# Performance work log

Measured on AMD Instinct MI355X. Metric: run time of the kernel, lower is better.

## Reference

```python
import jax, jax.numpy as jnp
import numpy as np

L = 8          # layers_num
G = 2 * L + 1  # grid side = 17
NH = 30        # n_hiper
D = 768
N = 4096       # ray samples


def setup_inputs() -> dict:
    key = jax.random.key(0)
    k1, k2, k3 = jax.random.split(key, 3)
    # coords must be in [-L, L) so shifted indices floor+1/ceil+1 stay in-bounds
    samples = jax.random.uniform(k1, (N, 3), minval=-float(L), maxval=float(L) - 1e-3)
    last_point = jax.random.uniform(k2, (3,), minval=-float(L), maxval=float(L) - 1e-3)
    embeddings = jax.random.normal(k3, (G, G, G, NH + 1, D), dtype=jnp.float32)
    return {"samples": samples, "last_point": last_point, "embeddings": embeddings}


def _interpolate(emb, samples):
    """Vectorized port of Text3DSpaceAll.interpolate for all N samples.
    emb: (G,G,G,NH+1,D); samples: (N,3). Returns (N, NH+1, D)."""
    Gs = emb.shape[0]
    p = samples + L                       # shift into [0, G-1)
    f = jnp.floor(p)
    c = jnp.ceil(p)
    d = p - f                             # fractional parts (same as pre-shift)
    fx, fy, fz = f[:, 0].astype(jnp.int32), f[:, 1].astype(jnp.int32), f[:, 2].astype(jnp.int32)
    cy, cz = c[:, 1].astype(jnp.int32), c[:, 2].astype(jnp.int32)
    dx, dy, dz = d[:, 0], d[:, 1], d[:, 2]

    def w(a):  # broadcast per-sample scalar over (NH+1, D)
        return a[:, None, None]

    def clip(i):
        return jnp.clip(i, 0, Gs - 1)

    def line(iy, iz):
        # 2-4 point stencil along x with boundary-dependent count
        g = lambda ix: emb[clip(ix), iy, iz]          # gather -> (N, NH+1, D)
        m_lo = (fx > 0).astype(dx.dtype)
        m_hi = (fx + 2 < Gs).astype(dx.dtype)
        out = (g(fx) * w(2.0 - dx) + g(fx + 1) * w(1.0 + dx)
               + g(fx - 1) * w((1.0 - dx) * m_lo)
               + g(fx + 2) * w(dx * m_hi))
        cnt = 2.0 + m_lo + m_hi
        return out / w(cnt)

    def plane(iz):
        m_lo = (fy > 0).astype(dy.dtype)
        m_hi = (fy + 2 < Gs).astype(dy.dtype)
        out = (line(fy, iz) * w(2.0 - dy) + line(cy, iz) * w(1.0 + dy)
               + line(clip(fy - 1), iz) * w((1.0 - dy) * m_lo)
               + line(clip(cy + 1), iz) * w(dy * m_hi))
        cnt = 2.0 + m_lo + m_hi
        return out / w(cnt)

    m_lo = (fz > 0).astype(dz.dtype)
    m_hi = (fz + 2 < Gs).astype(dz.dtype)
    out = (plane(fz) * w(2.0 - dz) + plane(cz) * w(1.0 + dz)
           + plane(clip(fz - 1)) * w((1.0 - dz) * m_lo)
           + plane(clip(cz + 1)) * w(dz * m_hi))
    cnt = 2.0 + m_lo + m_hi
    return out / w(cnt)


def reference(samples, last_point, embeddings):
    n_hiper = embeddings.shape[3] - 1
    interp = _interpolate(embeddings, samples)          # (N, NH+1, D)
    emb = interp[:, :n_hiper]                           # (N, NH, D)
    density = jax.nn.relu(interp[:, n_hiper])           # (N, D)
    # distance from each sample to the next (last one to last_point)
    nxt = jnp.concatenate([samples[1:], last_point[None]], axis=0)
    dists = jnp.linalg.norm(samples - nxt, axis=-1)     # (N,)
    sd = density * dists[:, None]                       # (N, D)
    # exclusive cumulative optical depth -> transmittance
    csum = jnp.cumsum(sd, axis=0)
    excl = jnp.concatenate([jnp.zeros_like(sd[:1]), csum[:-1]], axis=0)
    T = jnp.exp(-excl)
    alpha = 1.0 - jnp.exp(-sd)
    wgt = T * alpha                                     # (N, D)
    return jnp.einsum('nd,nhd->hd', wgt, emb)           # (NH, D)
```

## Files before the change

kernel.cpp:

```cpp
#include <hip/hip_runtime.h>
#include <math.h>

#define LL 8
#define G 17
#define NH 30
#define D 768
#define N 4096
#define CH 31
#define CELLS (G*G*G)
#define CSTRIDE (CH*D)
#define NBIN 16

__device__ __forceinline__ int iclip(int i){ return i<0?0:(i>G-1?G-1:i); }

__global__ void k_prep(const float* __restrict__ samples, const float* __restrict__ last_point,
                       float* __restrict__ wxyz, int* __restrict__ ixyz,
                       float* __restrict__ dist, int* __restrict__ sampleBin,
                       int* __restrict__ binCount){
    int s = blockIdx.x*blockDim.x + threadIdx.x;
    if (s >= N) return;
    float x0 = samples[s*3+0], y0 = samples[s*3+1], z0 = samples[s*3+2];
    float p[3] = {x0 + (float)LL, y0 + (float)LL, z0 + (float)LL};
    float fv[3], cv[3], dv[3]; int fi[3], ci[3];
    for (int a=0;a<3;a++){
        fv[a]=floorf(p[a]); cv[a]=ceilf(p[a]); dv[a]=p[a]-fv[a];
        fi[a]=(int)fv[a]; ci[a]=(int)cv[a];
    }
    {
        int fx=fi[0]; float dx=dv[0];
        float mlo=(fx>0)?1.f:0.f, mhi=(fx+2<G)?1.f:0.f;
        float cnt=2.f+mlo+mhi;
        float w[4]={(1.f-dx)*mlo/cnt,(2.f-dx)/cnt,(1.f+dx)/cnt,dx*mhi/cnt};
        int id[4]={iclip(fx-1),iclip(fx),iclip(fx+1),iclip(fx+2)};
        for(int i=0;i<4;i++){ wxyz[s*12+i]=w[i]; ixyz[s*12+i]=id[i]; }
    }
    {
        int fy=fi[1], cy=ci[1]; float dy=dv[1];
        float mlo=(fy>0)?1.f:0.f, mhi=(fy+2<G)?1.f:0.f;
        float cnt=2.f+mlo+mhi;
        float w[4]={(1.f-dy)*mlo/cnt,(2.f-dy)/cnt,(1.f+dy)/cnt,dy*mhi/cnt};
        int id[4]={iclip(fy-1),iclip(fy),iclip(cy),iclip(cy+1)};
        for(int i=0;i<4;i++){ wxyz[s*12+4+i]=w[i]; ixyz[s*12+4+i]=id[i]; }
    }
    {
        int fz=fi[2], cz=ci[2]; float dz=dv[2];
        float mlo=(fz>0)?1.f:0.f, mhi=(fz+2<G)?1.f:0.f;
        float cnt=2.f+mlo+mhi;
        float w[4]={(1.f-dz)*mlo/cnt,(2.f-dz)/cnt,(1.f+dz)/cnt,dz*mhi/cnt};
        int id[4]={iclip(fz-1),iclip(fz),iclip(cz),iclip(cz+1)};
        for(int i=0;i<4;i++){ wxyz[s*12+8+i]=w[i]; ixyz[s*12+8+i]=id[i]; }
    }
    float nx,ny,nz;
    if (s < N-1){ nx=samples[(s+1)*3+0]; ny=samples[(s+1)*3+1]; nz=samples[(s+1)*3+2]; }
    else        { nx=last_point[0];      ny=last_point[1];      nz=last_point[2]; }
    float ddx=x0-nx, ddy=y0-ny, ddz=z0-nz;
    dist[s]=sqrtf(ddx*ddx+ddy*ddy+ddz*ddz);
    int bx=min(max(fi[0],0),NBIN-1), by=min(max(fi[1],0),NBIN-1), bz=min(max(fi[2],0),NBIN-1);
    int bin=(bz*NBIN+by)*NBIN+bx;
    sampleBin[s]=bin;
    atomicAdd(&binCount[bin],1);
}

__global__ void k_binscan(const int* __restrict__ binCount, int* __restrict__ binStart,
                          int* __restrict__ binCursor){
    __shared__ int sh[256];
    __shared__ int srun;
    int t = threadIdx.x;
    if (t==0) srun=0;
    __syncthreads();
    for (int base=0; base<NBIN*NBIN*NBIN; base+=256){
        int v = binCount[base+t];
        sh[t]=v; __syncthreads();
        for (int off=1; off<256; off<<=1){
            int u = (t>=off)? sh[t-off] : 0;
            __syncthreads();
            sh[t]+=u;
            __syncthreads();
        }
        int incl = sh[t];
        int st = srun + incl - v;
        binStart[base+t]=st; binCursor[base+t]=st;
        __syncthreads();
        if (t==255) srun += incl;
        __syncthreads();
    }
}

__global__ void k_scatter(const int* __restrict__ sampleBin, int* __restrict__ binCursor,
                          int* __restrict__ binned){
    int s = blockIdx.x*blockDim.x + threadIdx.x;
    if (s>=N) return;
    int b=sampleBin[s];
    int pos=atomicAdd(&binCursor[b],1);
    binned[pos]=s;
}

__global__ __launch_bounds__(192) void k_density(const float* __restrict__ emb,
                       const float* __restrict__ wxyz, const int* __restrict__ ixyz,
                       const int* __restrict__ binned,
                       float* __restrict__ density){
    int b = blockIdx.x;
    int s = binned[((b & 7) << 9) | (b >> 3)];
    int t = threadIdx.x;
    __shared__ float w[12]; __shared__ int idx[12];
    if (t<12){ w[t]=wxyz[s*12+t]; idx[t]=ixyz[s*12+t]; }
    __syncthreads();
    float4 acc = make_float4(0.f,0.f,0.f,0.f);
    for (int i=0;i<4;i++){
        float wx=w[i]; if (wx==0.f) continue; int X=idx[i];
        for (int j=0;j<4;j++){
            float wxy=wx*w[4+j]; if (wxy==0.f) continue; int Y=idx[4+j];
            for (int k=0;k<4;k++){
                float www=wxy*w[8+k]; if (www==0.f) continue; int Z=idx[8+k];
                const float4* p = (const float4*)(emb + (size_t)((X*G+Y)*G+Z)*CSTRIDE + NH*D);
                float4 v = p[t];
                acc.x += www*v.x; acc.y += www*v.y; acc.z += www*v.z; acc.w += www*v.w;
            }
        }
    }
    ((float4*)(density + (size_t)s*D))[t] = acc;
}

__global__ void k_transpose(const float* __restrict__ in, float* __restrict__ out,
                            int R, int C){
    __shared__ float tile[64][65];
    int tx=threadIdx.x, ty=threadIdx.y;
    int c0=blockIdx.x*64, r0=blockIdx.y*64;
    #pragma unroll
    for (int k=0;k<16;k++){
        int r=r0+ty+k*4;
        tile[ty+k*4][tx] = in[(size_t)r*C + c0 + tx];
    }
    __syncthreads();
    #pragma unroll
    for (int k=0;k<16;k++){
        int c=c0+ty+k*4;
        out[(size_t)c*R + r0 + tx] = tile[tx][ty+k*4];
    }
}

__global__ void k_scan(const float* __restrict__ density_t, const float* __restrict__ dist,
                       float* __restrict__ wgt_t){
    int wave = threadIdx.x>>6, lane = threadIdx.x&63;
    int d = blockIdx.x*4 + wave;
    const float* col = density_t + (size_t)d*N;
    float* out = wgt_t + (size_t)d*N;
    float carry=0.f;
    for (int c0=0;c0<N;c0+=64){
        int n=c0+lane;
        float v=col[n];
        float sd=fmaxf(v,0.f)*dist[n];
        float x=sd;
        #pragma unroll
        for (int off=1; off<64; off<<=1){
            float u=__shfl_up(x,(unsigned)off,64);
            if (lane>=off) x+=u;
        }
        float incl=x+carry;
        out[n]=expf(sd-incl)-expf(-incl);
        carry=__shfl(incl,63,64);
    }
}

__global__ __launch_bounds__(192) void k_accumA(const float* __restrict__ wgt,
                       const float* __restrict__ wxyz, const int* __restrict__ ixyz,
                       const int* __restrict__ binStart, const int* __restrict__ binCount,
                       const int* __restrict__ binned, float* __restrict__ A){
    int b = blockIdx.x;
    int c = (b & 7) * 615 + (b >> 3);
    if (c >= CELLS) return;
    int t = threadIdx.x;
    int x=c/(G*G); int rem=c-x*G*G; int y=rem/G; int z=rem-y*G;
    float4 acc = make_float4(0.f,0.f,0.f,0.f);
    int bx0=max(0,x-2), bx1=min(NBIN-1,x+1);
    int by0=max(0,y-2), by1=min(NBIN-1,y+1);
    int bz0=max(0,z-2), bz1=min(NBIN-1,z+1);
    for (int bz=bz0;bz<=bz1;bz++)
    for (int by=by0;by<=by1;by++)
    for (int bx=bx0;bx<=bx1;bx++){
        int bin=(bz*NBIN+by)*NBIN+bx;
        int st=binStart[bin], cnt=binCount[bin];
        for (int q=0;q<cnt;q++){
            int s=binned[st+q];
            const float* w=wxyz+(size_t)s*12;
            const int* id=ixyz+(size_t)s*12;
            float px=0.f,py=0.f,pz=0.f;
            #pragma unroll
            for (int i=0;i<4;i++){
                px += (id[i]  ==x)? w[i]  :0.f;
                py += (id[4+i]==y)? w[4+i]:0.f;
                pz += (id[8+i]==z)? w[8+i]:0.f;
            }
            float wt=px*py*pz;
            if (wt!=0.f){
                const float4* wr=(const float4*)(wgt+(size_t)s*D);
                float4 v=wr[t];
                acc.x+=wt*v.x; acc.y+=wt*v.y; acc.z+=wt*v.z; acc.w+=wt*v.w;
            }
        }
    }
    ((float4*)(A+(size_t)c*D))[t]=acc;
}

#define CPG 32
__global__ __launch_bounds__(256) void k_out(const float* __restrict__ emb,
                      const float* __restrict__ A, float* __restrict__ out){
    int t=threadIdx.x;
    int d=blockIdx.y*256+t;
    int c0=blockIdx.x*CPG;
    int c1=min(CELLS,c0+CPG);
    float acc[NH];
    #pragma unroll
    for (int h=0;h<NH;h++) acc[h]=0.f;
    for (int c=c0;c<c1;c++){
        float a=A[(size_t)c*D+d];
        const float* e=emb+(size_t)c*CSTRIDE+d;
        #pragma unroll
        for (int h=0;h<NH;h++) acc[h]+=a*e[h*D];
    }
    #pragma unroll
    for (int h=0;h<NH;h++) atomicAdd(&out[h*D+d],acc[h]);
}

extern "C" void kernel_launch(void* const* d_in, const int* in_sizes, int n_in,
                              void* d_out, int out_size, void* d_ws, size_t ws_size,
                              hipStream_t stream){
    const float* samples   = (const float*)d_in[0];
    const float* last_point= (const float*)d_in[1];
    const float* emb       = (const float*)d_in[2];
    char* ws=(char*)d_ws;
    float* wxyz     =(float*)(ws + 0);
    int*   ixyz     =(int*)  (ws + 196608);
    float* dist     =(float*)(ws + 393216);
    int*   sampleBin=(int*)  (ws + 409600);
    int*   binCount =(int*)  (ws + 425984);
    int*   binStart =(int*)  (ws + 442368);
    int*   binCursor=(int*)  (ws + 458752);
    int*   binned   =(int*)  (ws + 475136);
    float* density  =(float*)(ws + 524288);
    float* density_t=(float*)(ws + 524288 + 12582912);
    float* wgt_t    =(float*)(ws + 524288 + 2*12582912);
    float* wgt      = density;
    float* A        =(float*)(ws + 524288 + 3*12582912);

    hipMemsetAsync(binCount, 0, 4096*sizeof(int), stream);
    hipMemsetAsync(d_out, 0, (size_t)out_size*sizeof(float), stream);

    k_prep   <<<N/256, 256, 0, stream>>>(samples, last_point, wxyz, ixyz, dist, sampleBin, binCount);
    k_binscan<<<1, 256, 0, stream>>>(binCount, binStart, binCursor);
    k_scatter<<<N/256, 256, 0, stream>>>(sampleBin, binCursor, binned);
    k_density<<<N, 192, 0, stream>>>(emb, wxyz, ixyz, binned, density);
    dim3 tb(64,4);
    k_transpose<<<dim3(D/64, N/64), tb, 0, stream>>>(density, density_t, N, D);
    k_scan   <<<D/4, 256, 0, stream>>>(density_t, dist, wgt_t);
    k_transpose<<<dim3(N/64, D/64), tb, 0, stream>>>(wgt_t, wgt, D, N);
    k_accumA <<<8*615, 192, 0, stream>>>(wgt, wxyz, ixyz, binStart, binCount, binned, A);
    k_out    <<<dim3((CELLS+CPG-1)/CPG, D/256), 256, 0, stream>>>(emb, A, (float*)d_out);
}
```

Before: 851.3 us.

## Parallelize column scan, precompute cell sample lists, replace output atomics with partial reduction

The per-column scan now gives each column its own block: the column is staged in padded shared memory, each thread scans 16 elements serially, and a wave plus block prefix combines the results, replacing the serial 64-wide loop. k_accumA first builds a shared list of contributing samples and weights, with the bin traversal spread across threads, so the per-sample weight test is no longer repeated by all 192 threads. k_out writes per-chunk partial sums that a new k_reduce kernel adds up, replacing the atomicAdds and the output memset. The trade-offs are more workspace traffic, an extra launch, and a silent truncation risk if a cell gets more than 1024 contributing samples.

```diff
diff --git a/kernel.cpp b/kernel.cpp
--- a/kernel.cpp
+++ b/kernel.cpp
@@ -10,6 +10,8 @@
 #define CELLS (G*G*G)
 #define CSTRIDE (CH*D)
 #define NBIN 16
+#define CPG 32
+#define NCHUNK ((CELLS+CPG-1)/CPG)
 
 __device__ __forceinline__ int iclip(int i){ return i<0?0:(i>G-1?G-1:i); }
 
@@ -139,29 +141,52 @@
     }
 }
 
-__global__ void k_scan(const float* __restrict__ density_t, const float* __restrict__ dist,
-                       float* __restrict__ wgt_t){
-    int wave = threadIdx.x>>6, lane = threadIdx.x&63;
-    int d = blockIdx.x*4 + wave;
+#define SIDX(n) ((n) + ((n)>>4))
+__global__ __launch_bounds__(256) void k_scan(const float* __restrict__ density_t,
+                       const float* __restrict__ dist, float* __restrict__ wgt_t){
+    __shared__ float buf[4096 + 256];
+    __shared__ float wtot[4];
+    int t = threadIdx.x;
+    int d = blockIdx.x;
     const float* col = density_t + (size_t)d*N;
     float* out = wgt_t + (size_t)d*N;
-    float carry=0.f;
-    for (int c0=0;c0<N;c0+=64){
-        int n=c0+lane;
-        float v=col[n];
-        float sd=fmaxf(v,0.f)*dist[n];
-        float x=sd;
-        #pragma unroll
-        for (int off=1; off<64; off<<=1){
-            float u=__shfl_up(x,(unsigned)off,64);
-            if (lane>=off) x+=u;
-        }
-        float incl=x+carry;
-        out[n]=expf(sd-incl)-expf(-incl);
-        carry=__shfl(incl,63,64);
-    }
-}
-
+    #pragma unroll
+    for (int i=0;i<16;i++){
+        int n = i*256 + t;
+        buf[SIDX(n)] = fmaxf(col[n], 0.f) * dist[n];
+    }
+    __syncthreads();
+    int lane = t & 63, wave = t >> 6;
+    float vals[16]; float sum = 0.f;
+    #pragma unroll
+    for (int j=0;j<16;j++){ vals[j] = buf[SIDX(t*16+j)]; sum += vals[j]; }
+    float x = sum;
+    #pragma unroll
+    for (int off=1; off<64; off<<=1){
+        float u = __shfl_up(x, (unsigned)off, 64);
+        if (lane >= off) x += u;
+    }
+    if (lane == 63) wtot[wave] = x;
+    float thread_excl = x - sum;
+    __syncthreads();
+    float wexcl = 0.f;
+    for (int w2=0; w2<4; w2++) if (w2 < wave) wexcl += wtot[w2];
+    float run = wexcl + thread_excl;
+    #pragma unroll
+    for (int j=0;j<16;j++){
+        float sd = vals[j];
+        run += sd;
+        buf[SIDX(t*16+j)] = expf(sd-run) - expf(-run);
+    }
+    __syncthreads();
+    #pragma unroll
+    for (int i=0;i<16;i++){
+        int n = i*256 + t;
+        out[n] = buf[SIDX(n)];
+    }
+}
+
+#define MAXS 1024
 __global__ __launch_bounds__(192) void k_accumA(const float* __restrict__ wgt,
                        const float* __restrict__ wxyz, const int* __restrict__ ixyz,
                        const int* __restrict__ binStart, const int* __restrict__ binCount,
@@ -171,19 +196,25 @@
     if (c >= CELLS) return;
     int t = threadIdx.x;
     int x=c/(G*G); int rem=c-x*G*G; int y=rem/G; int z=rem-y*G;
-    float4 acc = make_float4(0.f,0.f,0.f,0.f);
+    __shared__ int   ls[MAXS];
+    __shared__ float lw[MAXS];
+    __shared__ int   lcount;
+    if (t==0) lcount = 0;
+    __syncthreads();
     int bx0=max(0,x-2), bx1=min(NBIN-1,x+1);
     int by0=max(0,y-2), by1=min(NBIN-1,y+1);
     int bz0=max(0,z-2), bz1=min(NBIN-1,z+1);
-    for (int bz=bz0;bz<=bz1;bz++)
-    for (int by=by0;by<=by1;by++)
-    for (int bx=bx0;bx<=bx1;bx++){
-        int bin=(bz*NBIN+by)*NBIN+bx;
-        int st=binStart[bin], cnt=binCount[bin];
+    int nx=bx1-bx0+1, ny=by1-by0+1, nz=bz1-bz0+1;
+    int nb = nx*ny*nz;
+    for (int bi=t; bi<nb; bi+=192){
+        int bxo = bi % nx; int r2 = bi / nx;
+        int byo = r2 % ny; int bzo = r2 / ny;
+        int bin = ((bz0+bzo)*NBIN + (by0+byo))*NBIN + (bx0+bxo);
+        int st = binStart[bin], cnt = binCount[bin];
         for (int q=0;q<cnt;q++){
-            int s=binned[st+q];
-            const float* w=wxyz+(size_t)s*12;
-            const int* id=ixyz+(size_t)s*12;
+            int s = binned[st+q];
+            const float* w = wxyz + (size_t)s*12;
+            const int* id  = ixyz + (size_t)s*12;
             float px=0.f,py=0.f,pz=0.f;
             #pragma unroll
             for (int i=0;i<4;i++){
@@ -191,23 +222,30 @@
                 py += (id[4+i]==y)? w[4+i]:0.f;
                 pz += (id[8+i]==z)? w[8+i]:0.f;
             }
-            float wt=px*py*pz;
-            if (wt!=0.f){
-                const float4* wr=(const float4*)(wgt+(size_t)s*D);
-                float4 v=wr[t];
-                acc.x+=wt*v.x; acc.y+=wt*v.y; acc.z+=wt*v.z; acc.w+=wt*v.w;
+            float wt = px*py*pz;
+            if (wt != 0.f){
+                int pos = atomicAdd(&lcount, 1);
+                if (pos < MAXS){ ls[pos]=s; lw[pos]=wt; }
             }
         }
     }
-    ((float4*)(A+(size_t)c*D))[t]=acc;
-}
-
-#define CPG 32
+    __syncthreads();
+    int m = min(lcount, MAXS);
+    float4 acc = make_float4(0.f,0.f,0.f,0.f);
+    for (int i=0;i<m;i++){
+        int s = ls[i]; float wt = lw[i];
+        float4 v = ((const float4*)(wgt + (size_t)s*D))[t];
+        acc.x += wt*v.x; acc.y += wt*v.y; acc.z += wt*v.z; acc.w += wt*v.w;
+    }
+    ((float4*)(A + (size_t)c*D))[t] = acc;
+}
+
 __global__ __launch_bounds__(256) void k_out(const float* __restrict__ emb,
-                      const float* __restrict__ A, float* __restrict__ out){
+                      const float* __restrict__ A, float* __restrict__ partial){
     int t=threadIdx.x;
     int d=blockIdx.y*256+t;
-    int c0=blockIdx.x*CPG;
+    int chunk=blockIdx.x;
+    int c0=chunk*CPG;
     int c1=min(CELLS,c0+CPG);
     float acc[NH];
     #pragma unroll
@@ -218,8 +256,18 @@
         #pragma unroll
         for (int h=0;h<NH;h++) acc[h]+=a*e[h*D];
     }
-    #pragma unroll
-    for (int h=0;h<NH;h++) atomicAdd(&out[h*D+d],acc[h]);
+    float* pr = partial + (size_t)chunk*NH*D + d;
+    #pragma unroll
+    for (int h=0;h<NH;h++) pr[h*D] = acc[h];
+}
+
+__global__ __launch_bounds__(256) void k_reduce(const float* __restrict__ partial,
+                       float* __restrict__ out){
+    int i = blockIdx.x*256 + threadIdx.x;
+    if (i >= NH*D) return;
+    float s = 0.f;
+    for (int c=0;c<NCHUNK;c++) s += partial[(size_t)c*NH*D + i];
+    out[i] = s;
 }
 
 extern "C" void kernel_launch(void* const* d_in, const int* in_sizes, int n_in,
@@ -242,9 +290,9 @@
     float* wgt_t    =(float*)(ws + 524288 + 2*12582912);
     float* wgt      = density;
     float* A        =(float*)(ws + 524288 + 3*12582912);
+    float* partial  =(float*)(ws + 524288 + 3*12582912 + 15093504);
 
     hipMemsetAsync(binCount, 0, 4096*sizeof(int), stream);
-    hipMemsetAsync(d_out, 0, (size_t)out_size*sizeof(float), stream);
 
     k_prep   <<<N/256, 256, 0, stream>>>(samples, last_point, wxyz, ixyz, dist, sampleBin, binCount);
     k_binscan<<<1, 256, 0, stream>>>(binCount, binStart, binCursor);
@@ -252,8 +300,9 @@
     k_density<<<N, 192, 0, stream>>>(emb, wxyz, ixyz, binned, density);
     dim3 tb(64,4);
     k_transpose<<<dim3(D/64, N/64), tb, 0, stream>>>(density, density_t, N, D);
-    k_scan   <<<D/4, 256, 0, stream>>>(density_t, dist, wgt_t);
+    k_scan   <<<D, 256, 0, stream>>>(density_t, dist, wgt_t);
     k_transpose<<<dim3(N/64, D/64), tb, 0, stream>>>(wgt_t, wgt, D, N);
     k_accumA <<<8*615, 192, 0, stream>>>(wgt, wxyz, ixyz, binStart, binCount, binned, A);
-    k_out    <<<dim3((CELLS+CPG-1)/CPG, D/256), 256, 0, stream>>>(emb, A, (float*)d_out);
-}
+    k_out    <<<dim3(NCHUNK, D/256), 256, 0, stream>>>(emb, A, partial);
+    k_reduce <<<(NH*D+255)/256, 256, 0, stream>>>(partial, (float*)d_out);
+}
```

Result: faster. 750.9 us (-11.8%).
